# Kernel optimization log

Hardware: AMD Instinct MI355X
Metric: run time of the kernel (lower is better)

The kernel has to match this reference:

```python
import jax, jax.numpy as jnp
import numpy as np

B, C, H, W = 4, 512, 64, 64
D = C // 8  # inter_channels = 64


def setup_inputs() -> dict:
    key = jax.random.key(0)
    ks = jax.random.split(key, 10)
    s = 1.0 / np.sqrt(C)
    so = 1.0 / np.sqrt(D)
    return {
        "x": jax.random.normal(ks[0], (B, C, H, W), dtype=jnp.float32),
        "Wq": jax.random.normal(ks[1], (D, C), dtype=jnp.float32) * s,
        "bq": jnp.zeros((D,), dtype=jnp.float32),
        "Wk": jax.random.normal(ks[2], (D, C), dtype=jnp.float32) * s,
        "bk": jnp.zeros((D,), dtype=jnp.float32),
        "Wv": jax.random.normal(ks[3], (D, C), dtype=jnp.float32) * s,
        "bv": jnp.zeros((D,), dtype=jnp.float32),
        "Wo": jax.random.normal(ks[4], (C, D), dtype=jnp.float32) * so,
        "bo": jnp.zeros((C,), dtype=jnp.float32),
        "gamma": jnp.zeros((1,), dtype=jnp.float32),
    }


def reference(x, Wq, bq, Wk, bk, Wv, bv, Wo, bo, gamma):
    b, c, h, w = x.shape
    n = h * w
    xf = x.reshape(b, c, n)  # (B, C, N)
    # 1x1 convs == channel-mixing matmuls
    q = jnp.einsum("dc,bcn->bnd", Wq, xf) + bq              # (B, N, D)
    k = jnp.einsum("dc,bcn->bdn", Wk, xf) + bk[:, None]      # (B, D, N)
    v = jnp.einsum("dc,bcn->bnd", Wv, xf) + bv               # (B, N, D)
    scores = jnp.einsum("bnd,bdm->bnm", q, k)                # (B, N, N)
    weights = jax.nn.softmax(scores, axis=-1)
    attended = jnp.einsum("bnm,bmd->bnd", weights, v)        # (B, N, D)
    out = jnp.einsum("cd,bnd->bcn", Wo, attended) + bo[:, None]
    out = out.reshape(b, c, h, w)
    return gamma[0] * out + x
```

## Files before the change

kernel.cpp:

```cpp
#include <hip/hip_runtime.h>

#define NB 4
#define CH 512
#define NN 4096
#define DD 64

typedef __attribute__((ext_vector_type(8))) short bf16x8;
typedef __attribute__((ext_vector_type(4))) float f32x4;

#define MFMA(a, b, c) __builtin_amdgcn_mfma_f32_16x16x32_bf16((a), (b), (c), 0, 0, 0)

__device__ inline unsigned short f2bf(float f) {
    unsigned int u = __builtin_bit_cast(unsigned int, f);
    unsigned int r = u + 0x7fffu + ((u >> 16) & 1u);
    return (unsigned short)(r >> 16);
}

__device__ inline float bf2f(unsigned short u) {
    return __builtin_bit_cast(float, ((unsigned int)u) << 16);
}

__device__ inline bf16x8 ld8(const unsigned short* p) {
    return *reinterpret_cast<const bf16x8*>(p);
}

__global__ __launch_bounds__(256) void convert_w(
    const float* __restrict__ Wq, const float* __restrict__ Wk,
    const float* __restrict__ Wv, const float* __restrict__ Wo,
    unsigned short* __restrict__ oq, unsigned short* __restrict__ ok,
    unsigned short* __restrict__ ov, unsigned short* __restrict__ oo) {
    int i = blockIdx.x * 256 + threadIdx.x;
    oq[i] = f2bf(Wq[i]);
    ok[i] = f2bf(Wk[i]);
    ov[i] = f2bf(Wv[i]);
    oo[i] = f2bf(Wo[i]);
}

__global__ __launch_bounds__(256) void qkv_kernel(
    const float* __restrict__ x,
    const unsigned short* __restrict__ Wq, const unsigned short* __restrict__ Wk,
    const unsigned short* __restrict__ Wv,
    const float* __restrict__ bq, const float* __restrict__ bk, const float* __restrict__ bv,
    unsigned short* __restrict__ Q, unsigned short* __restrict__ K,
    unsigned short* __restrict__ VT) {
    const int b = blockIdx.x >> 6;
    const int n0 = (blockIdx.x & 63) * 64;
    const int t = threadIdx.x;
    const int lane = t & 63, w = t >> 6;
    const int l15 = lane & 15, g = lane >> 4;
    const int nn = t & 63, ccb = (t >> 6) * 16;

    __shared__ unsigned short sxT[64][72];

    f32x4 accQ[4], accK[4], accV[4];
    const f32x4 z = {0.f, 0.f, 0.f, 0.f};
#pragma unroll
    for (int i = 0; i < 4; ++i) { accQ[i] = z; accK[i] = z; accV[i] = z; }

    float rv[16];
#pragma unroll
    for (int p = 0; p < 16; ++p)
        rv[p] = x[((b * CH + ccb + p) * NN) + n0 + nn];

    for (int c0 = 0; c0 < CH; c0 += 64) {
        __syncthreads();
#pragma unroll
        for (int p = 0; p < 16; ++p)
            sxT[nn][ccb + p] = f2bf(rv[p]);
        __syncthreads();
        if (c0 + 64 < CH) {
#pragma unroll
            for (int p = 0; p < 16; ++p)
                rv[p] = x[((b * CH + c0 + 64 + ccb + p) * NN) + n0 + nn];
        }
#pragma unroll
        for (int kk = 0; kk < 2; ++kk) {
            bf16x8 ax = ld8(&sxT[16 * w + l15][kk * 32 + 8 * g]);
            int c = c0 + kk * 32 + 8 * g;
#pragma unroll
            for (int dt = 0; dt < 4; ++dt) {
                int d = dt * 16 + l15;
                bf16x8 wq = ld8(&Wq[d * CH + c]);
                accQ[dt] = MFMA(ax, wq, accQ[dt]);
                bf16x8 wk = ld8(&Wk[d * CH + c]);
                accK[dt] = MFMA(ax, wk, accK[dt]);
                bf16x8 wv = ld8(&Wv[d * CH + c]);
                accV[dt] = MFMA(wv, ax, accV[dt]);
            }
        }
    }

#pragma unroll
    for (int dt = 0; dt < 4; ++dt) {
        int d = dt * 16 + l15;
        float biasq = bq[d], biask = bk[d];
#pragma unroll
        for (int r = 0; r < 4; ++r) {
            int n = n0 + 16 * w + 4 * g + r;
            Q[(b * NN + n) * DD + d] = f2bf(accQ[dt][r] + biasq);
            K[(b * NN + n) * DD + d] = f2bf(accK[dt][r] + biask);
        }
    }
#pragma unroll
    for (int dt = 0; dt < 4; ++dt) {
#pragma unroll
        for (int r = 0; r < 4; ++r) {
            int d = dt * 16 + 4 * g + r;
            VT[(b * DD + d) * NN + n0 + 16 * w + l15] = f2bf(accV[dt][r] + bv[d]);
        }
    }
}

__global__ __launch_bounds__(256) void attn_kernel(
    const unsigned short* __restrict__ Q, const unsigned short* __restrict__ K,
    const unsigned short* __restrict__ VT,
    unsigned short* __restrict__ PO, float* __restrict__ PML, int KVLEN) {
    const int s = blockIdx.x >> 8;
    const int bq_ = blockIdx.x & 255;
    const int b = bq_ >> 6;
    const int n0 = (bq_ & 63) * 64;
    const int t = threadIdx.x;
    const int lane = t & 63, w = t >> 6;
    const int l15 = lane & 15, g = lane >> 4;

    __shared__ unsigned short sK[64][72];
    __shared__ unsigned short sVT[64][72];
    __shared__ unsigned short sP[4][16][72];

    const int qrow = n0 + 16 * w + l15;
    bf16x8 qf0 = ld8(&Q[(b * NN + qrow) * DD + 0 + 8 * g]);
    bf16x8 qf1 = ld8(&Q[(b * NN + qrow) * DD + 32 + 8 * g]);

    f32x4 oacc[4];
    const f32x4 z = {0.f, 0.f, 0.f, 0.f};
#pragma unroll
    for (int i = 0; i < 4; ++i) oacc[i] = z;
    float m_run[4], l_run[4];
#pragma unroll
    for (int r = 0; r < 4; ++r) { m_run[r] = -1e30f; l_run[r] = 0.f; }

    const int kv_begin = s * KVLEN;
    const int kv_end = kv_begin + KVLEN;
    for (int m0 = kv_begin; m0 < kv_end; m0 += 64) {
        {
            int row = t >> 2, c16 = (t & 3) * 16;
            const unsigned short* kp = &K[(b * NN + m0 + row) * DD + c16];
            *reinterpret_cast<bf16x8*>(&sK[row][c16]) = ld8(kp);
            *reinterpret_cast<bf16x8*>(&sK[row][c16 + 8]) = ld8(kp + 8);
            const unsigned short* vp = &VT[(b * DD + row) * NN + m0 + c16];
            *reinterpret_cast<bf16x8*>(&sVT[row][c16]) = ld8(vp);
            *reinterpret_cast<bf16x8*>(&sVT[row][c16 + 8]) = ld8(vp + 8);
        }
        __syncthreads();

        f32x4 sv[4];
#pragma unroll
        for (int ct = 0; ct < 4; ++ct) sv[ct] = z;
#pragma unroll
        for (int ct = 0; ct < 4; ++ct) {
            bf16x8 kf0 = ld8(&sK[ct * 16 + l15][0 + 8 * g]);
            sv[ct] = MFMA(qf0, kf0, sv[ct]);
            bf16x8 kf1 = ld8(&sK[ct * 16 + l15][32 + 8 * g]);
            sv[ct] = MFMA(qf1, kf1, sv[ct]);
        }

        float corr[4];
#pragma unroll
        for (int r = 0; r < 4; ++r) {
            float mx = fmaxf(fmaxf(sv[0][r], sv[1][r]), fmaxf(sv[2][r], sv[3][r]));
#pragma unroll
            for (int d_ = 8; d_ >= 1; d_ >>= 1) mx = fmaxf(mx, __shfl_xor(mx, d_, 64));
            float mnew = fmaxf(m_run[r], mx);
            float c_ = __expf(m_run[r] - mnew);
            float rs = 0.f;
#pragma unroll
            for (int ct = 0; ct < 4; ++ct) {
                float p = __expf(sv[ct][r] - mnew);
                sv[ct][r] = p;
                rs += p;
            }
#pragma unroll
            for (int d_ = 8; d_ >= 1; d_ >>= 1) rs += __shfl_xor(rs, d_, 64);
            l_run[r] = l_run[r] * c_ + rs;
            m_run[r] = mnew;
            corr[r] = c_;
        }
#pragma unroll
        for (int dt = 0; dt < 4; ++dt)
#pragma unroll
            for (int r = 0; r < 4; ++r) oacc[dt][r] *= corr[r];

#pragma unroll
        for (int ct = 0; ct < 4; ++ct)
#pragma unroll
            for (int r = 0; r < 4; ++r)
                sP[w][4 * g + r][ct * 16 + l15] = f2bf(sv[ct][r]);

#pragma unroll
        for (int kk = 0; kk < 2; ++kk) {
            bf16x8 pf = ld8(&sP[w][l15][kk * 32 + 8 * g]);
#pragma unroll
            for (int dt = 0; dt < 4; ++dt) {
                bf16x8 vf = ld8(&sVT[dt * 16 + l15][kk * 32 + 8 * g]);
                oacc[dt] = MFMA(pf, vf, oacc[dt]);
            }
        }
        __syncthreads();
    }

#pragma unroll
    for (int r = 0; r < 4; ++r) {
        int n = n0 + 16 * w + 4 * g + r;
        size_t rowidx = (size_t)s * NB * NN + (size_t)b * NN + n;
#pragma unroll
        for (int dt = 0; dt < 4; ++dt)
            PO[rowidx * DD + dt * 16 + l15] = f2bf(oacc[dt][r]);
        if (l15 == 0) {
            PML[rowidx * 2 + 0] = m_run[r];
            PML[rowidx * 2 + 1] = l_run[r];
        }
    }
}

__global__ __launch_bounds__(256) void attn_combine(
    const unsigned short* __restrict__ PO, const float* __restrict__ PML,
    unsigned short* __restrict__ ATT, int S) {
    const int t = threadIdx.x;
    const int R = blockIdx.x * 64 + (t >> 2);
    const int dq = (t & 3) * 16;

    float m = -1e30f;
    for (int s = 0; s < S; ++s) m = fmaxf(m, PML[((size_t)s * NB * NN + R) * 2]);

    float acc[16];
#pragma unroll
    for (int j = 0; j < 16; ++j) acc[j] = 0.f;
    float l = 0.f;
    for (int s = 0; s < S; ++s) {
        size_t rowidx = (size_t)s * NB * NN + R;
        float ms = PML[rowidx * 2 + 0];
        float ls = PML[rowidx * 2 + 1];
        float wgt = __expf(ms - m);
        l += wgt * ls;
        bf16x8 a0 = ld8(&PO[rowidx * DD + dq]);
        bf16x8 a1 = ld8(&PO[rowidx * DD + dq + 8]);
#pragma unroll
        for (int j = 0; j < 8; ++j) {
            acc[j] += wgt * bf2f((unsigned short)a0[j]);
            acc[8 + j] += wgt * bf2f((unsigned short)a1[j]);
        }
    }
    float inv = 1.f / l;
    bf16x8 o0, o1;
#pragma unroll
    for (int j = 0; j < 8; ++j) {
        o0[j] = (short)f2bf(acc[j] * inv);
        o1[j] = (short)f2bf(acc[8 + j] * inv);
    }
    *reinterpret_cast<bf16x8*>(&ATT[(size_t)R * DD + dq]) = o0;
    *reinterpret_cast<bf16x8*>(&ATT[(size_t)R * DD + dq + 8]) = o1;
}

__global__ __launch_bounds__(256) void out_kernel(
    const unsigned short* __restrict__ Wo, const unsigned short* __restrict__ ATT,
    const float* __restrict__ bo, const float* __restrict__ gamma,
    const float* __restrict__ x, float* __restrict__ out) {
    const int bid = blockIdx.x;
    const int b = bid >> 8;
    const int rest = bid & 255;
    const int n0 = (rest >> 2) * 64;
    const int c0 = (rest & 3) * 128;
    const int t = threadIdx.x;
    const int lane = t & 63, w = t >> 6;
    const int l15 = lane & 15, g = lane >> 4;
    const int cw = c0 + w * 32;

    f32x4 acc[2][4];
    const f32x4 z = {0.f, 0.f, 0.f, 0.f};
#pragma unroll
    for (int i = 0; i < 2; ++i)
#pragma unroll
        for (int j = 0; j < 4; ++j) acc[i][j] = z;

#pragma unroll
    for (int kk = 0; kk < 2; ++kk) {
        bf16x8 af[2], bfr[4];
#pragma unroll
        for (int ct = 0; ct < 2; ++ct)
            af[ct] = ld8(&Wo[(cw + ct * 16 + l15) * DD + kk * 32 + 8 * g]);
#pragma unroll
        for (int nt = 0; nt < 4; ++nt)
            bfr[nt] = ld8(&ATT[((size_t)b * NN + n0 + nt * 16 + l15) * DD + kk * 32 + 8 * g]);
#pragma unroll
        for (int ct = 0; ct < 2; ++ct)
#pragma unroll
            for (int nt = 0; nt < 4; ++nt) acc[ct][nt] = MFMA(af[ct], bfr[nt], acc[ct][nt]);
    }

    float gm = gamma[0];
#pragma unroll
    for (int ct = 0; ct < 2; ++ct) {
        int c = cw + ct * 16 + 4 * g;
#pragma unroll
        for (int r = 0; r < 4; ++r) {
            float bias = bo[c + r];
#pragma unroll
            for (int nt = 0; nt < 4; ++nt) {
                int n = n0 + nt * 16 + l15;
                int idx = (b * CH + c + r) * NN + n;
                out[idx] = gm * (acc[ct][nt][r] + bias) + x[idx];
            }
        }
    }
}

extern "C" void kernel_launch(void* const* d_in, const int* in_sizes, int n_in,
                              void* d_out, int out_size, void* d_ws, size_t ws_size,
                              hipStream_t stream) {
    const float* x = (const float*)d_in[0];
    const float* Wq = (const float*)d_in[1];
    const float* bq = (const float*)d_in[2];
    const float* Wk = (const float*)d_in[3];
    const float* bk = (const float*)d_in[4];
    const float* Wv = (const float*)d_in[5];
    const float* bv = (const float*)d_in[6];
    const float* Wo = (const float*)d_in[7];
    const float* bo = (const float*)d_in[8];
    const float* gamma = (const float*)d_in[9];
    float* out = (float*)d_out;

    char* ws = (char*)d_ws;
    unsigned short* Wq_bf = (unsigned short*)(ws + 0);
    unsigned short* Wk_bf = (unsigned short*)(ws + 65536);
    unsigned short* Wv_bf = (unsigned short*)(ws + 131072);
    unsigned short* Wo_bf = (unsigned short*)(ws + 196608);
    unsigned short* Qb = (unsigned short*)(ws + 262144);
    unsigned short* Kb = (unsigned short*)(ws + 262144 + 2097152);
    unsigned short* VTb = (unsigned short*)(ws + 262144 + 2 * 2097152);
    unsigned short* ATTb = (unsigned short*)(ws + 262144 + 3 * 2097152);
    size_t po_off = 262144 + 4 * 2097152;

    size_t need4 = po_off + 4ull * ((size_t)NB * NN * DD * 2 + (size_t)NB * NN * 8);
    int S = (ws_size >= need4) ? 4 : 1;
    unsigned short* PO = (unsigned short*)(ws + po_off);
    float* PML = (float*)(ws + po_off + (size_t)S * NB * NN * DD * 2);

    hipLaunchKernelGGL(convert_w, dim3(128), dim3(256), 0, stream,
                       Wq, Wk, Wv, Wo, Wq_bf, Wk_bf, Wv_bf, Wo_bf);
    hipLaunchKernelGGL(qkv_kernel, dim3(256), dim3(256), 0, stream,
                       x, Wq_bf, Wk_bf, Wv_bf, bq, bk, bv, Qb, Kb, VTb);
    hipLaunchKernelGGL(attn_kernel, dim3(256 * S), dim3(256), 0, stream,
                       Qb, Kb, VTb, PO, PML, NN / S);
    hipLaunchKernelGGL(attn_combine, dim3(NB * NN / 64), dim3(256), 0, stream,
                       PO, PML, ATTb, S);
    hipLaunchKernelGGL(out_kernel, dim3(1024), dim3(256), 0, stream,
                       Wo_bf, ATTb, bo, gamma, x, out);
}
```

Baseline: 217.5 us.

## Fuse split-KV combine into output projection, reshape QKV grid, raise split count

Restructures the QKV projection to use 1024 blocks of 16 tokens, each loading the full channel slice into shared memory once and splitting channels across waves with a shared-memory reduction. The separate combine kernel is folded into the output projection, so the merged attention tile stays in shared memory instead of going through a global ATT buffer. The number of KV splits rises to 8 when workspace allows, and the sP row padding changes to reduce bank conflicts. This saves a launch and a global round trip and gives more parallelism, at the cost of redundant combine work across the four channel blocks that share a token tile and more partial-output traffic.

```diff
diff --git a/kernel.cpp b/kernel.cpp
--- a/kernel.cpp
+++ b/kernel.cpp
@@ -43,70 +43,91 @@
     const float* __restrict__ bq, const float* __restrict__ bk, const float* __restrict__ bv,
     unsigned short* __restrict__ Q, unsigned short* __restrict__ K,
     unsigned short* __restrict__ VT) {
-    const int b = blockIdx.x >> 6;
-    const int n0 = (blockIdx.x & 63) * 64;
+    const int b = blockIdx.x >> 8;
+    const int n0 = (blockIdx.x & 255) * 16;
     const int t = threadIdx.x;
     const int lane = t & 63, w = t >> 6;
     const int l15 = lane & 15, g = lane >> 4;
-    const int nn = t & 63, ccb = (t >> 6) * 16;
-
-    __shared__ unsigned short sxT[64][72];
+
+    __shared__ char smraw[36864];
+    unsigned short (*sxT)[520] = (unsigned short(*)[520])smraw;
+    float* red = (float*)smraw;
+
+    {
+        const int cbase = t >> 2;
+        const int nq = (t & 3) * 4;
+#pragma unroll
+        for (int p = 0; p < 8; ++p) {
+            int c = p * 64 + cbase;
+            float4 v = *reinterpret_cast<const float4*>(
+                &x[((size_t)(b * CH + c)) * NN + n0 + nq]);
+            sxT[nq + 0][c] = f2bf(v.x);
+            sxT[nq + 1][c] = f2bf(v.y);
+            sxT[nq + 2][c] = f2bf(v.z);
+            sxT[nq + 3][c] = f2bf(v.w);
+        }
+    }
+    __syncthreads();
 
     f32x4 accQ[4], accK[4], accV[4];
     const f32x4 z = {0.f, 0.f, 0.f, 0.f};
 #pragma unroll
     for (int i = 0; i < 4; ++i) { accQ[i] = z; accK[i] = z; accV[i] = z; }
 
-    float rv[16];
-#pragma unroll
-    for (int p = 0; p < 16; ++p)
-        rv[p] = x[((b * CH + ccb + p) * NN) + n0 + nn];
-
-    for (int c0 = 0; c0 < CH; c0 += 64) {
-        __syncthreads();
-#pragma unroll
-        for (int p = 0; p < 16; ++p)
-            sxT[nn][ccb + p] = f2bf(rv[p]);
-        __syncthreads();
-        if (c0 + 64 < CH) {
-#pragma unroll
-            for (int p = 0; p < 16; ++p)
-                rv[p] = x[((b * CH + c0 + 64 + ccb + p) * NN) + n0 + nn];
-        }
-#pragma unroll
-        for (int kk = 0; kk < 2; ++kk) {
-            bf16x8 ax = ld8(&sxT[16 * w + l15][kk * 32 + 8 * g]);
-            int c = c0 + kk * 32 + 8 * g;
-#pragma unroll
-            for (int dt = 0; dt < 4; ++dt) {
-                int d = dt * 16 + l15;
-                bf16x8 wq = ld8(&Wq[d * CH + c]);
-                accQ[dt] = MFMA(ax, wq, accQ[dt]);
-                bf16x8 wk = ld8(&Wk[d * CH + c]);
-                accK[dt] = MFMA(ax, wk, accK[dt]);
-                bf16x8 wv = ld8(&Wv[d * CH + c]);
-                accV[dt] = MFMA(wv, ax, accV[dt]);
-            }
-        }
-    }
-
-#pragma unroll
-    for (int dt = 0; dt < 4; ++dt) {
-        int d = dt * 16 + l15;
-        float biasq = bq[d], biask = bk[d];
-#pragma unroll
-        for (int r = 0; r < 4; ++r) {
-            int n = n0 + 16 * w + 4 * g + r;
-            Q[(b * NN + n) * DD + d] = f2bf(accQ[dt][r] + biasq);
-            K[(b * NN + n) * DD + d] = f2bf(accK[dt][r] + biask);
-        }
-    }
-#pragma unroll
-    for (int dt = 0; dt < 4; ++dt) {
-#pragma unroll
-        for (int r = 0; r < 4; ++r) {
-            int d = dt * 16 + 4 * g + r;
-            VT[(b * DD + d) * NN + n0 + 16 * w + l15] = f2bf(accV[dt][r] + bv[d]);
+    const int wc = w * 128;
+#pragma unroll
+    for (int i = 0; i < 4; ++i) {
+        int c = wc + i * 32 + 8 * g;
+        bf16x8 ax = ld8(&sxT[l15][c]);
+#pragma unroll
+        for (int dt = 0; dt < 4; ++dt) {
+            int d = dt * 16 + l15;
+            accQ[dt] = MFMA(ax, ld8(&Wq[d * CH + c]), accQ[dt]);
+            accK[dt] = MFMA(ax, ld8(&Wk[d * CH + c]), accK[dt]);
+            accV[dt] = MFMA(ld8(&Wv[d * CH + c]), ax, accV[dt]);
+        }
+    }
+    __syncthreads();
+
+    if (w > 0) {
+        float* dst = &red[((w - 1) * 64 + lane) * 48];
+#pragma unroll
+        for (int i = 0; i < 4; ++i) {
+            *reinterpret_cast<f32x4*>(&dst[i * 4]) = accQ[i];
+            *reinterpret_cast<f32x4*>(&dst[16 + i * 4]) = accK[i];
+            *reinterpret_cast<f32x4*>(&dst[32 + i * 4]) = accV[i];
+        }
+    }
+    __syncthreads();
+    if (w == 0) {
+#pragma unroll
+        for (int ww = 0; ww < 3; ++ww) {
+            const float* src = &red[(ww * 64 + lane) * 48];
+#pragma unroll
+            for (int i = 0; i < 4; ++i) {
+                accQ[i] += *reinterpret_cast<const f32x4*>(&src[i * 4]);
+                accK[i] += *reinterpret_cast<const f32x4*>(&src[16 + i * 4]);
+                accV[i] += *reinterpret_cast<const f32x4*>(&src[32 + i * 4]);
+            }
+        }
+#pragma unroll
+        for (int dt = 0; dt < 4; ++dt) {
+            int d = dt * 16 + l15;
+            float biasq = bq[d], biask = bk[d];
+#pragma unroll
+            for (int r = 0; r < 4; ++r) {
+                int n = n0 + 4 * g + r;
+                Q[((size_t)b * NN + n) * DD + d] = f2bf(accQ[dt][r] + biasq);
+                K[((size_t)b * NN + n) * DD + d] = f2bf(accK[dt][r] + biask);
+            }
+        }
+#pragma unroll
+        for (int dt = 0; dt < 4; ++dt) {
+#pragma unroll
+            for (int r = 0; r < 4; ++r) {
+                int d = dt * 16 + 4 * g + r;
+                VT[((size_t)b * DD + d) * NN + n0 + l15] = f2bf(accV[dt][r] + bv[d]);
+            }
         }
     }
 }
@@ -125,11 +146,11 @@
 
     __shared__ unsigned short sK[64][72];
     __shared__ unsigned short sVT[64][72];
-    __shared__ unsigned short sP[4][16][72];
+    __shared__ unsigned short sP[4][16][76];
 
     const int qrow = n0 + 16 * w + l15;
-    bf16x8 qf0 = ld8(&Q[(b * NN + qrow) * DD + 0 + 8 * g]);
-    bf16x8 qf1 = ld8(&Q[(b * NN + qrow) * DD + 32 + 8 * g]);
+    bf16x8 qf0 = ld8(&Q[((size_t)b * NN + qrow) * DD + 0 + 8 * g]);
+    bf16x8 qf1 = ld8(&Q[((size_t)b * NN + qrow) * DD + 32 + 8 * g]);
 
     f32x4 oacc[4];
     const f32x4 z = {0.f, 0.f, 0.f, 0.f};
@@ -144,10 +165,10 @@
     for (int m0 = kv_begin; m0 < kv_end; m0 += 64) {
         {
             int row = t >> 2, c16 = (t & 3) * 16;
-            const unsigned short* kp = &K[(b * NN + m0 + row) * DD + c16];
+            const unsigned short* kp = &K[((size_t)b * NN + m0 + row) * DD + c16];
             *reinterpret_cast<bf16x8*>(&sK[row][c16]) = ld8(kp);
             *reinterpret_cast<bf16x8*>(&sK[row][c16 + 8]) = ld8(kp + 8);
-            const unsigned short* vp = &VT[(b * DD + row) * NN + m0 + c16];
+            const unsigned short* vp = &VT[((size_t)b * DD + row) * NN + m0 + c16];
             *reinterpret_cast<bf16x8*>(&sVT[row][c16]) = ld8(vp);
             *reinterpret_cast<bf16x8*>(&sVT[row][c16 + 8]) = ld8(vp + 8);
         }
@@ -222,49 +243,11 @@
     }
 }
 
-__global__ __launch_bounds__(256) void attn_combine(
-    const unsigned short* __restrict__ PO, const float* __restrict__ PML,
-    unsigned short* __restrict__ ATT, int S) {
-    const int t = threadIdx.x;
-    const int R = blockIdx.x * 64 + (t >> 2);
-    const int dq = (t & 3) * 16;
-
-    float m = -1e30f;
-    for (int s = 0; s < S; ++s) m = fmaxf(m, PML[((size_t)s * NB * NN + R) * 2]);
-
-    float acc[16];
-#pragma unroll
-    for (int j = 0; j < 16; ++j) acc[j] = 0.f;
-    float l = 0.f;
-    for (int s = 0; s < S; ++s) {
-        size_t rowidx = (size_t)s * NB * NN + R;
-        float ms = PML[rowidx * 2 + 0];
-        float ls = PML[rowidx * 2 + 1];
-        float wgt = __expf(ms - m);
-        l += wgt * ls;
-        bf16x8 a0 = ld8(&PO[rowidx * DD + dq]);
-        bf16x8 a1 = ld8(&PO[rowidx * DD + dq + 8]);
-#pragma unroll
-        for (int j = 0; j < 8; ++j) {
-            acc[j] += wgt * bf2f((unsigned short)a0[j]);
-            acc[8 + j] += wgt * bf2f((unsigned short)a1[j]);
-        }
-    }
-    float inv = 1.f / l;
-    bf16x8 o0, o1;
-#pragma unroll
-    for (int j = 0; j < 8; ++j) {
-        o0[j] = (short)f2bf(acc[j] * inv);
-        o1[j] = (short)f2bf(acc[8 + j] * inv);
-    }
-    *reinterpret_cast<bf16x8*>(&ATT[(size_t)R * DD + dq]) = o0;
-    *reinterpret_cast<bf16x8*>(&ATT[(size_t)R * DD + dq + 8]) = o1;
-}
-
-__global__ __launch_bounds__(256) void out_kernel(
-    const unsigned short* __restrict__ Wo, const unsigned short* __restrict__ ATT,
-    const float* __restrict__ bo, const float* __restrict__ gamma,
-    const float* __restrict__ x, float* __restrict__ out) {
+__global__ __launch_bounds__(256) void out_fused(
+    const unsigned short* __restrict__ Wo, const unsigned short* __restrict__ PO,
+    const float* __restrict__ PML, const float* __restrict__ bo,
+    const float* __restrict__ gamma, const float* __restrict__ x,
+    float* __restrict__ out, int S) {
     const int bid = blockIdx.x;
     const int b = bid >> 8;
     const int rest = bid & 255;
@@ -273,14 +256,53 @@
     const int t = threadIdx.x;
     const int lane = t & 63, w = t >> 6;
     const int l15 = lane & 15, g = lane >> 4;
+
+    __shared__ unsigned short sATT[64][72];
+
+    {
+        const int row = t >> 2;
+        const int dq = (t & 3) * 16;
+        const size_t base = (size_t)b * NN + n0 + row;
+        float m = -1e30f;
+        for (int s = 0; s < S; ++s)
+            m = fmaxf(m, PML[((size_t)s * NB * NN + base) * 2]);
+        float acc[16];
+#pragma unroll
+        for (int j = 0; j < 16; ++j) acc[j] = 0.f;
+        float l = 0.f;
+        for (int s = 0; s < S; ++s) {
+            size_t rowidx = (size_t)s * NB * NN + base;
+            float ms = PML[rowidx * 2 + 0];
+            float ls = PML[rowidx * 2 + 1];
+            float wgt = __expf(ms - m);
+            l += wgt * ls;
+            bf16x8 a0 = ld8(&PO[rowidx * DD + dq]);
+            bf16x8 a1 = ld8(&PO[rowidx * DD + dq + 8]);
+#pragma unroll
+            for (int j = 0; j < 8; ++j) {
+                acc[j] += wgt * bf2f((unsigned short)a0[j]);
+                acc[8 + j] += wgt * bf2f((unsigned short)a1[j]);
+            }
+        }
+        float inv = 1.f / l;
+        bf16x8 o0, o1;
+#pragma unroll
+        for (int j = 0; j < 8; ++j) {
+            o0[j] = (short)f2bf(acc[j] * inv);
+            o1[j] = (short)f2bf(acc[8 + j] * inv);
+        }
+        *reinterpret_cast<bf16x8*>(&sATT[row][dq]) = o0;
+        *reinterpret_cast<bf16x8*>(&sATT[row][dq + 8]) = o1;
+    }
+    __syncthreads();
+
     const int cw = c0 + w * 32;
-
-    f32x4 acc[2][4];
+    f32x4 acc2[2][4];
     const f32x4 z = {0.f, 0.f, 0.f, 0.f};
 #pragma unroll
     for (int i = 0; i < 2; ++i)
 #pragma unroll
-        for (int j = 0; j < 4; ++j) acc[i][j] = z;
+        for (int j = 0; j < 4; ++j) acc2[i][j] = z;
 
 #pragma unroll
     for (int kk = 0; kk < 2; ++kk) {
@@ -290,11 +312,11 @@
             af[ct] = ld8(&Wo[(cw + ct * 16 + l15) * DD + kk * 32 + 8 * g]);
 #pragma unroll
         for (int nt = 0; nt < 4; ++nt)
-            bfr[nt] = ld8(&ATT[((size_t)b * NN + n0 + nt * 16 + l15) * DD + kk * 32 + 8 * g]);
+            bfr[nt] = ld8(&sATT[nt * 16 + l15][kk * 32 + 8 * g]);
 #pragma unroll
         for (int ct = 0; ct < 2; ++ct)
 #pragma unroll
-            for (int nt = 0; nt < 4; ++nt) acc[ct][nt] = MFMA(af[ct], bfr[nt], acc[ct][nt]);
+            for (int nt = 0; nt < 4; ++nt) acc2[ct][nt] = MFMA(af[ct], bfr[nt], acc2[ct][nt]);
     }
 
     float gm = gamma[0];
@@ -307,8 +329,8 @@
 #pragma unroll
             for (int nt = 0; nt < 4; ++nt) {
                 int n = n0 + nt * 16 + l15;
-                int idx = (b * CH + c + r) * NN + n;
-                out[idx] = gm * (acc[ct][nt][r] + bias) + x[idx];
+                size_t idx = ((size_t)b * CH + c + r) * NN + n;
+                out[idx] = gm * (acc2[ct][nt][r] + bias) + x[idx];
             }
         }
     }
@@ -337,22 +359,21 @@
     unsigned short* Qb = (unsigned short*)(ws + 262144);
     unsigned short* Kb = (unsigned short*)(ws + 262144 + 2097152);
     unsigned short* VTb = (unsigned short*)(ws + 262144 + 2 * 2097152);
-    unsigned short* ATTb = (unsigned short*)(ws + 262144 + 3 * 2097152);
-    size_t po_off = 262144 + 4 * 2097152;
-
-    size_t need4 = po_off + 4ull * ((size_t)NB * NN * DD * 2 + (size_t)NB * NN * 8);
-    int S = (ws_size >= need4) ? 4 : 1;
+    const size_t po_off = 262144 + 3ull * 2097152;
+
+    int S = 8;
+    while (S > 1 &&
+           ws_size < po_off + (size_t)S * (2097152ull + 131072ull))
+        S >>= 1;
     unsigned short* PO = (unsigned short*)(ws + po_off);
-    float* PML = (float*)(ws + po_off + (size_t)S * NB * NN * DD * 2);
+    float* PML = (float*)(ws + po_off + (size_t)S * 2097152ull);
 
     hipLaunchKernelGGL(convert_w, dim3(128), dim3(256), 0, stream,
                        Wq, Wk, Wv, Wo, Wq_bf, Wk_bf, Wv_bf, Wo_bf);
-    hipLaunchKernelGGL(qkv_kernel, dim3(256), dim3(256), 0, stream,
+    hipLaunchKernelGGL(qkv_kernel, dim3(1024), dim3(256), 0, stream,
                        x, Wq_bf, Wk_bf, Wv_bf, bq, bk, bv, Qb, Kb, VTb);
     hipLaunchKernelGGL(attn_kernel, dim3(256 * S), dim3(256), 0, stream,
                        Qb, Kb, VTb, PO, PML, NN / S);
-    hipLaunchKernelGGL(attn_combine, dim3(NB * NN / 64), dim3(256), 0, stream,
-                       PO, PML, ATTb, S);
-    hipLaunchKernelGGL(out_kernel, dim3(1024), dim3(256), 0, stream,
-                       Wo_bf, ATTb, bo, gamma, x, out);
-}
+    hipLaunchKernelGGL(out_fused, dim3(1024), dim3(256), 0, stream,
+                       Wo_bf, PO, PML, bo, gamma, x, out, S);
+}
```

Result: no change. 214.4 us (-1.4%).
